# Kernel tuning notes

Hardware: AMD Instinct MI355X
Metric: run time of the kernel (lower is better)

The kernel has to match this reference:

```python
import jax, jax.numpy as jnp
import numpy as np

B, N, D, DH = 2, 512, 64, 64


def _lin_params(key, din, dout):
    kw, kb = jax.random.split(key)
    bound = 1.0 / np.sqrt(din)
    W = jax.random.uniform(kw, (din, dout), jnp.float32, -bound, bound)
    b = jax.random.uniform(kb, (dout,), jnp.float32, -bound, bound)
    return W, b


def setup_inputs() -> dict:
    key = jax.random.key(0)
    ks = jax.random.split(key, 11)
    inp = {
        "x": jax.random.normal(ks[0], (B, N, D), jnp.float32),
        "e": jax.random.normal(ks[1], (B, N, N, D), jnp.float32),
    }
    # node-to-node self-attention: Linear(d, d_head)
    inp["Wq1"], inp["bq1"] = _lin_params(ks[2], D, DH)
    inp["Wk1"], inp["bk1"] = _lin_params(ks[3], D, DH)
    inp["Wv1"], inp["bv1"] = _lin_params(ks[4], D, DH)
    # node-to-edge cross-attention
    inp["Wqe"], inp["bqe"] = _lin_params(ks[5], D, DH)   # Q_edge: Linear(d, d_head) on e
    inp["Wkn"], inp["bkn"] = _lin_params(ks[6], DH, DH)  # K_node: Linear(d_head, d_head)
    inp["Wvn"], inp["bvn"] = _lin_params(ks[7], DH, DH)  # V_node
    # edge-to-node cross-attention (all Linear(d_head, d_head))
    inp["Wqn"], inp["bqn"] = _lin_params(ks[8], DH, DH)
    inp["Wke"], inp["bke"] = _lin_params(ks[9], DH, DH)
    inp["Wve"], inp["bve"] = _lin_params(ks[10], DH, DH)
    return inp


def _forward(x, e, Wq1, bq1, Wk1, bk1, Wv1, bv1,
             Wqe, bqe, Wkn, bkn, Wvn, bvn,
             Wqn, bqn, Wke, bke, Wve, bve):
    sqrt_d = jnp.sqrt(jnp.asarray(DH, x.dtype))
    lin = lambda z, W, b: z @ W + b

    # --- self-attention node-to-node: x (B,N,d) -> x_hat (B,N,d_head) ---
    Q = lin(x, Wq1, bq1)
    K = lin(x, Wk1, bk1)
    V = lin(x, Wv1, bv1)
    A = jax.nn.softmax(jnp.einsum('bnd,bmd->bnm', Q, K) / sqrt_d, axis=-1)
    x_hat = jnp.einsum('bnm,bmd->bnd', A, V)

    # --- cross-attention node-to-edge: update e (B,N,N,d) -> e_new (B,N,N,d_head) ---
    Qe = lin(e, Wqe, bqe)                 # (B,N,N,dh)
    Kn = lin(x_hat, Wkn, bkn)             # (B,N,dh)
    Vn = lin(x_hat, Wvn, bvn)
    Si = jnp.einsum('bijd,bjd->bij', Qe, Kn) / sqrt_d  # K_i[b,i,j] = Kn[b,j]
    Sj = jnp.einsum('bijd,bid->bij', Qe, Kn) / sqrt_d  # K_j[b,i,j] = Kn[b,i]
    # Att_i/(Att_i+Att_j) = sigmoid(Si - Sj)
    Ai = jax.nn.sigmoid(Si - Sj)
    Aj = 1.0 - Ai
    e_new = Ai[..., None] * Vn[:, None, :, :] + Aj[..., None] * Vn[:, :, None, :]

    # --- cross-attention edge-to-node: x_new (B,N,d_head) ---
    Qn = lin(x_hat, Wqn, bqn)             # (B,N,dh)
    Ke = lin(e_new, Wke, bke)             # (B,N,N,dh)
    Ve = lin(e_new, Wve, bve)
    S = jnp.einsum('bid,bijd->bij', Qn, Ke) / sqrt_d
    A2 = jax.nn.softmax(S, axis=2)
    x_new = jnp.einsum('bij,bijd->bid', A2, Ve)
    return x_new, e_new


def reference(x, e, Wq1, bq1, Wk1, bk1, Wv1, bv1,
              Wqe, bqe, Wkn, bkn, Wvn, bvn,
              Wqn, bqn, Wke, bke, Wve, bve):
    return _forward(x, e, Wq1, bq1, Wk1, bk1, Wv1, bv1,
                    Wqe, bqe, Wkn, bkn, Wvn, bvn,
                    Wqn, bqn, Wke, bke, Wve, bve)
```

## Files before the change

### kernel.cpp

```cpp
#include <hip/hip_runtime.h>
#include <math.h>

#define NN 512

typedef float f4 __attribute__((ext_vector_type(4)));

__global__ __launch_bounds__(256) void prep_kernel(
    const float* __restrict__ x,
    const float* __restrict__ Wq1, const float* __restrict__ bq1,
    const float* __restrict__ Wk1, const float* __restrict__ bk1,
    const float* __restrict__ Wv1, const float* __restrict__ bv1,
    const float* __restrict__ Wkn, const float* __restrict__ bkn,
    const float* __restrict__ Wvn, const float* __restrict__ bvn,
    const float* __restrict__ Wqe, const float* __restrict__ bqe,
    const float* __restrict__ Wke, const float* __restrict__ Wve,
    float* __restrict__ Q, float* __restrict__ K, float* __restrict__ V,
    float* __restrict__ M_P, float* __restrict__ c_P,
    float* __restrict__ M_ke, float* __restrict__ c_ke,
    float* __restrict__ M_ve, float* __restrict__ c_ve,
    float* __restrict__ vq0, float* __restrict__ s0p)
{
    __shared__ float sh[14528];
    const int t = threadIdx.x;

    if (blockIdx.x < 3) {
        const int m = blockIdx.x;
        float* As = sh;
        float* Bs = sh + 4160;
        float* va = sh + 8320;
        float* vb = sh + 8384;
        const float* A  = (m == 0) ? Wkn : Wvn;
        const float* aV = (m == 0) ? bkn : bvn;
        const float* B  = (m == 0) ? Wqe : (m == 1 ? Wke : Wve);
#pragma unroll
        for (int p = 0; p < 16; ++p) {
            const int idx = p * 256 + t;
            const int r = idx >> 6, cc = idx & 63;
            As[r * 65 + cc] = A[idx];
            if (m == 0) Bs[r * 65 + cc] = B[idx];
            else        Bs[cc * 65 + r] = B[idx];
        }
        if (t < 64) { va[t] = aV[t]; vb[t] = bqe[t]; }
        __syncthreads();

        const int b = t & 63, g = t >> 6;
        float acc[16];
#pragma unroll
        for (int aa = 0; aa < 16; ++aa) acc[aa] = 0.f;
        for (int k = 0; k < 64; ++k) {
            const float bv = Bs[b * 65 + k];
#pragma unroll
            for (int aa = 0; aa < 16; ++aa)
                acc[aa] = fmaf(As[(g * 16 + aa) * 65 + k], bv, acc[aa]);
        }
        float* M = (m == 0) ? M_P : (m == 1 ? M_ke : M_ve);
#pragma unroll
        for (int aa = 0; aa < 16; ++aa)
            M[(g * 16 + aa) * 64 + b] = acc[aa];

        if (t < 64) {
            float cb = 0.f;
            for (int k = 0; k < 64; ++k) cb = fmaf(va[k], Bs[t * 65 + k], cb);
            float* C = (m == 0) ? c_P : (m == 1 ? c_ke : c_ve);
            C[t] = cb;
            if (m == 0) {
                float q = 0.f;
                for (int k = 0; k < 64; ++k) q = fmaf(As[t * 65 + k], vb[k], q);
                vq0[t] = q * 0.125f;
            }
        }
        if (m == 0 && t == 0) {
            float s = 0.f;
            for (int k = 0; k < 64; ++k) s += vb[k] * va[k];
            *s0p = s * 0.125f;
        }
    } else {
        const int rb = (blockIdx.x - 3) * 32;
        float* Ws0 = sh;
        float* Ws1 = sh + 4096;
        float* Ws2 = sh + 8192;
        float* xs  = sh + 12288;
        float* bs0 = sh + 14336;
        float* bs1 = sh + 14400;
        float* bs2 = sh + 14464;
#pragma unroll
        for (int p = 0; p < 4; ++p) {
            const int idx = p * 256 + t;
            ((f4*)Ws0)[idx] = ((const f4*)Wq1)[idx];
            ((f4*)Ws1)[idx] = ((const f4*)Wk1)[idx];
            ((f4*)Ws2)[idx] = ((const f4*)Wv1)[idx];
        }
        ((f4*)xs)[t]       = ((const f4*)(x + rb * 64))[t];
        ((f4*)xs)[t + 256] = ((const f4*)(x + rb * 64))[t + 256];
        if (t < 64) { bs0[t] = bq1[t]; bs1[t] = bk1[t]; bs2[t] = bv1[t]; }
        __syncthreads();

        const int d = t & 63, g = t >> 6;
        float a0[8], a1[8], a2[8];
#pragma unroll
        for (int r = 0; r < 8; ++r) { a0[r] = bs0[d]; a1[r] = bs1[d]; a2[r] = bs2[d]; }
        for (int k4 = 0; k4 < 16; ++k4) {
            float w0[4], w1[4], w2[4];
#pragma unroll
            for (int kk = 0; kk < 4; ++kk) {
                w0[kk] = Ws0[(k4 * 4 + kk) * 64 + d];
                w1[kk] = Ws1[(k4 * 4 + kk) * 64 + d];
                w2[kk] = Ws2[(k4 * 4 + kk) * 64 + d];
            }
#pragma unroll
            for (int r = 0; r < 8; ++r) {
                const f4 xv = ((const f4*)xs)[(g * 8 + r) * 16 + k4];
                a0[r] = fmaf(xv.x, w0[0], fmaf(xv.y, w0[1], fmaf(xv.z, w0[2], fmaf(xv.w, w0[3], a0[r]))));
                a1[r] = fmaf(xv.x, w1[0], fmaf(xv.y, w1[1], fmaf(xv.z, w1[2], fmaf(xv.w, w1[3], a1[r]))));
                a2[r] = fmaf(xv.x, w2[0], fmaf(xv.y, w2[1], fmaf(xv.z, w2[2], fmaf(xv.w, w2[3], a2[r]))));
            }
        }
#pragma unroll
        for (int r = 0; r < 8; ++r) {
            Q[(rb + g * 8 + r) * 64 + d] = a0[r];
            K[(rb + g * 8 + r) * 64 + d] = a1[r];
            V[(rb + g * 8 + r) * 64 + d] = a2[r];
        }
    }
}

__global__ __launch_bounds__(512) void selfattn_kernel(
    const float* __restrict__ Q, const float* __restrict__ K,
    const float* __restrict__ V, float* __restrict__ xhat)
{
    const int row = blockIdx.x;
    const int b = row >> 9;
    const int t = threadIdx.x;
    __shared__ float qr[64];
    __shared__ float p[512];
    __shared__ float red[512];
    if (t < 64) qr[t] = Q[row * 64 + t];
    __syncthreads();

    {
        const int m = t;
        const f4* kr = (const f4*)(K + (size_t)(b * NN + m) * 64);
        const f4* qq = (const f4*)qr;
        float sp[4] = {0.f, 0.f, 0.f, 0.f};
#pragma unroll
        for (int u = 0; u < 16; ++u) {
            const f4 w = kr[u];
            const f4 qv = qq[u];
            sp[u & 3] += qv.x * w.x + qv.y * w.y + qv.z * w.z + qv.w * w.w;
        }
        p[m] = ((sp[0] + sp[1]) + (sp[2] + sp[3])) * 0.125f;
    }
    __syncthreads();

    const int lane = t & 63, w = t >> 6;
    const float v0 = p[t];
    float m = v0;
#pragma unroll
    for (int o = 1; o < 64; o <<= 1) m = fmaxf(m, __shfl_xor(m, o));
    if (lane == 0) red[w] = m;
    __syncthreads();
    float mx = red[0];
#pragma unroll
    for (int z = 1; z < 8; ++z) mx = fmaxf(mx, red[z]);
    const float e0 = expf(v0 - mx);
    float ss = e0;
#pragma unroll
    for (int o = 1; o < 64; o <<= 1) ss += __shfl_xor(ss, o);
    if (lane == 0) red[8 + w] = ss;
    __syncthreads();
    const float inv = 1.f / (red[8] + red[9] + red[10] + red[11]
                           + red[12] + red[13] + red[14] + red[15]);
    p[t] = e0;
    __syncthreads();

    const int d = t & 63, q = t >> 6;
    float acc = 0.f;
    const int j0 = q * 64;
    for (int j = j0; j < j0 + 64; ++j)
        acc = fmaf(p[j], V[(b * NN + j) * 64 + d], acc);
    red[t] = acc;
    __syncthreads();
    if (t < 64) {
        float s8 = 0.f;
#pragma unroll
        for (int z = 0; z < 8; ++z) s8 += red[t + z * 64];
        xhat[row * 64 + t] = s8 * inv;
    }
}

__global__ __launch_bounds__(256) void affine5_kernel(
    const float* __restrict__ xhat,
    const float* __restrict__ Wqn, const float* __restrict__ bqn,
    const float* __restrict__ Wvn, const float* __restrict__ bvn,
    const float* __restrict__ M_P, const float* __restrict__ c_P,
    const float* __restrict__ M_ke, const float* __restrict__ c_ke,
    const float* __restrict__ M_ve, const float* __restrict__ c_ve,
    const float* __restrict__ vq0, const float* __restrict__ s0p,
    float* __restrict__ Qn, float* __restrict__ Vn, float* __restrict__ P,
    float* __restrict__ VnWke, float* __restrict__ VnWve, float* __restrict__ q0)
{
    const int t = threadIdx.x;
    const int rb = blockIdx.x * 32;
    const int m = blockIdx.y;
    const float* W; const float* c; float* o;
    if (m == 0)      { W = Wqn;  c = bqn;  o = Qn; }
    else if (m == 1) { W = Wvn;  c = bvn;  o = Vn; }
    else if (m == 2) { W = M_P;  c = c_P;  o = P; }
    else if (m == 3) { W = M_ke; c = c_ke; o = VnWke; }
    else             { W = M_ve; c = c_ve; o = VnWve; }
    __shared__ float Ws[4096], xs[2048], cs[64], vq0s[64];
#pragma unroll
    for (int p = 0; p < 4; ++p) ((f4*)Ws)[p * 256 + t] = ((const f4*)W)[p * 256 + t];
    ((f4*)xs)[t]       = ((const f4*)(xhat + rb * 64))[t];
    ((f4*)xs)[t + 256] = ((const f4*)(xhat + rb * 64))[t + 256];
    if (t < 64) { cs[t] = c[t]; if (m == 0) vq0s[t] = vq0[t]; }
    __syncthreads();

    const int d = t & 63, g = t >> 6;
    float acc[8];
#pragma unroll
    for (int r = 0; r < 8; ++r) acc[r] = cs[d];
    for (int k4 = 0; k4 < 16; ++k4) {
        float w[4];
#pragma unroll
        for (int kk = 0; kk < 4; ++kk) w[kk] = Ws[(k4 * 4 + kk) * 64 + d];
#pragma unroll
        for (int r = 0; r < 8; ++r) {
            const f4 xv = ((const f4*)xs)[(g * 8 + r) * 16 + k4];
            acc[r] = fmaf(xv.x, w[0], fmaf(xv.y, w[1], fmaf(xv.z, w[2], fmaf(xv.w, w[3], acc[r]))));
        }
    }
#pragma unroll
    for (int r = 0; r < 8; ++r) o[(rb + g * 8 + r) * 64 + d] = acc[r];

    if (m == 0) {
        const int row = t >> 3, seg = t & 7;
        float part = 0.f;
#pragma unroll
        for (int kk = 0; kk < 8; ++kk)
            part = fmaf(xs[row * 64 + seg * 8 + kk], vq0s[seg * 8 + kk], part);
        part += __shfl_xor(part, 1);
        part += __shfl_xor(part, 2);
        part += __shfl_xor(part, 4);
        if (seg == 0) q0[rb + row] = part + s0p[0];
    }
}

__global__ __launch_bounds__(256) void edgenode_kernel(
    const float* __restrict__ e, const float* __restrict__ P,
    const float* __restrict__ q0, const float* __restrict__ Vn,
    const float* __restrict__ Qn, const float* __restrict__ VnWke,
    const float* __restrict__ VnWve, const float* __restrict__ bve,
    float* __restrict__ e_new, float* __restrict__ x_new)
{
    const int bi = blockIdx.x;
    const int b = bi >> 9, i = bi & 511;
    const int t = threadIdx.x;
    const int r = t >> 4;
    const int k = t & 15;

    __shared__ float qn[64], pis[64], vis[64];
    __shared__ float as_[512], us[512], cs[512], q0s[512];
    __shared__ float red[256];

    if (t < 64) {
        qn[t]  = Qn[bi * 64 + t];
        pis[t] = P[bi * 64 + t];
        vis[t] = Vn[bi * 64 + t];
    }
    q0s[t]       = q0[b * NN + t];
    q0s[t + 256] = q0[b * NN + t + 256];
    __syncthreads();
    const float q0i = q0s[i];
    const float4 pi4 = ((const float4*)pis)[k];
    const float4 vi4 = ((const float4*)vis)[k];
    const float4 qn4 = ((const float4*)qn)[k];

    const f4* erow  = (const f4*)(e     + (size_t)bi * NN * 64);
    f4*       enrow = (f4*)      (e_new + (size_t)bi * NN * 64);

    for (int c0 = 0; c0 < 32; ++c0) {
        const int j  = c0 * 16 + r;
        const int bj = b * NN + j;
        const f4 ev = erow[j * 16 + k];
        const float4 pj = ((const float4*)P)[bj * 16 + k];
        const float4 wj = ((const float4*)VnWke)[bj * 16 + k];
        float s = ev.x * (pj.x - pi4.x) + ev.y * (pj.y - pi4.y)
                + ev.z * (pj.z - pi4.z) + ev.w * (pj.w - pi4.w);
        float uu = qn4.x * wj.x + qn4.y * wj.y + qn4.z * wj.z + qn4.w * wj.w;
        s  += __shfl_xor(s, 1);  uu += __shfl_xor(uu, 1);
        s  += __shfl_xor(s, 2);  uu += __shfl_xor(uu, 2);
        s  += __shfl_xor(s, 4);  uu += __shfl_xor(uu, 4);
        s  += __shfl_xor(s, 8);  uu += __shfl_xor(uu, 8);
        const float ai = 1.f / (1.f + expf(-(s * 0.125f + q0s[j] - q0i)));
        const float4 vj = ((const float4*)Vn)[bj * 16 + k];
        f4 en;
        en.x = fmaf(ai, vj.x - vi4.x, vi4.x);
        en.y = fmaf(ai, vj.y - vi4.y, vi4.y);
        en.z = fmaf(ai, vj.z - vi4.z, vi4.z);
        en.w = fmaf(ai, vj.w - vi4.w, vi4.w);
        __builtin_nontemporal_store(en, enrow + j * 16 + k);
        if (k == 0) { as_[j] = ai; us[j] = uu * 0.125f; }
    }
    __syncthreads();

    const int lane = t & 63, w = t >> 6;
    const float uii = us[i];
    const float v0 = as_[t] * (us[t] - uii);
    const float v1 = as_[t + 256] * (us[t + 256] - uii);
    float m = fmaxf(v0, v1);
#pragma unroll
    for (int o = 1; o < 64; o <<= 1) m = fmaxf(m, __shfl_xor(m, o));
    if (lane == 0) red[w] = m;
    __syncthreads();
    const float mx = fmaxf(fmaxf(red[0], red[1]), fmaxf(red[2], red[3]));
    const float e0 = expf(v0 - mx), e1 = expf(v1 - mx);
    float ss = e0 + e1;
#pragma unroll
    for (int o = 1; o < 64; o <<= 1) ss += __shfl_xor(ss, o);
    if (lane == 0) red[4 + w] = ss;
    __syncthreads();
    const float inv = 1.f / (red[4] + red[5] + red[6] + red[7]);
    const float c0v = e0 * inv * as_[t];
    const float c1v = e1 * inv * as_[t + 256];
    cs[t] = c0v; cs[t + 256] = c1v;
    float gg = c0v + c1v;
#pragma unroll
    for (int o = 1; o < 64; o <<= 1) gg += __shfl_xor(gg, o);
    if (lane == 0) red[8 + w] = gg;
    __syncthreads();
    const float g = red[8] + red[9] + red[10] + red[11];
    __syncthreads();

    const int d = t & 63, q = t >> 6;
    float acc = 0.f;
    const int j0 = q * 128;
    for (int j = j0; j < j0 + 128; ++j)
        acc = fmaf(cs[j], VnWve[(b * NN + j) * 64 + d], acc);
    red[t] = acc;
    __syncthreads();
    if (t < 64) {
        const float s4 = red[t] + red[t + 64] + red[t + 128] + red[t + 192];
        x_new[bi * 64 + t] = bve[t] + VnWve[bi * 64 + t] * (1.f - g) + s4;
    }
}

extern "C" void kernel_launch(void* const* d_in, const int* in_sizes, int n_in,
                              void* d_out, int out_size, void* d_ws, size_t ws_size,
                              hipStream_t stream) {
    const float* x   = (const float*)d_in[0];
    const float* e   = (const float*)d_in[1];
    const float* Wq1 = (const float*)d_in[2];  const float* bq1 = (const float*)d_in[3];
    const float* Wk1 = (const float*)d_in[4];  const float* bk1 = (const float*)d_in[5];
    const float* Wv1 = (const float*)d_in[6];  const float* bv1 = (const float*)d_in[7];
    const float* Wqe = (const float*)d_in[8];  const float* bqe = (const float*)d_in[9];
    const float* Wkn = (const float*)d_in[10]; const float* bkn = (const float*)d_in[11];
    const float* Wvn = (const float*)d_in[12]; const float* bvn = (const float*)d_in[13];
    const float* Wqn = (const float*)d_in[14]; const float* bqn = (const float*)d_in[15];
    const float* Wke = (const float*)d_in[16];
    const float* Wve = (const float*)d_in[18]; const float* bve = (const float*)d_in[19];

    float* out = (float*)d_out;
    float* x_new = out;
    float* e_new = out + 2 * NN * 64;

    float* ws = (float*)d_ws;
    const int R = 2 * NN;
    float* Q     = ws;
    float* K     = Q + R * 64;
    float* V     = K + R * 64;
    float* xhat  = V + R * 64;
    float* Qn    = xhat + R * 64;
    float* Vn    = Qn + R * 64;
    float* P     = Vn + R * 64;
    float* VnWke = P + R * 64;
    float* VnWve = VnWke + R * 64;
    float* q0    = VnWve + R * 64;
    float* M_P   = q0 + R;
    float* M_ke  = M_P + 4096;
    float* M_ve  = M_ke + 4096;
    float* c_P   = M_ve + 4096;
    float* c_ke  = c_P + 64;
    float* c_ve  = c_ke + 64;
    float* vq0   = c_ve + 64;
    float* s0    = vq0 + 64;

    prep_kernel<<<35, 256, 0, stream>>>(x, Wq1, bq1, Wk1, bk1, Wv1, bv1,
                                        Wkn, bkn, Wvn, bvn, Wqe, bqe, Wke, Wve,
                                        Q, K, V,
                                        M_P, c_P, M_ke, c_ke, M_ve, c_ve, vq0, s0);
    selfattn_kernel<<<R, 512, 0, stream>>>(Q, K, V, xhat);
    affine5_kernel<<<dim3(32, 5), 256, 0, stream>>>(xhat, Wqn, bqn, Wvn, bvn,
                                                    M_P, c_P, M_ke, c_ke, M_ve, c_ve,
                                                    vq0, s0,
                                                    Qn, Vn, P, VnWke, VnWve, q0);
    edgenode_kernel<<<R, 256, 0, stream>>>(e, P, q0, Vn, Qn, VnWke, VnWve, bve,
                                           e_new, x_new);
}
```

Baseline: 97.91 us.

## Split edge kernel over j-chunks and finish softmax reduction in a separate kernel

The per-row edge kernel is split into 8 blocks per (b,i), each handling 64 columns j. The softmax over j is computed without max subtraction, so partial exp sums, gated sums and weighted VnWve sums can be accumulated per chunk and combined by a small final kernel. This gives eight times more blocks to hide memory latency on the large e stream and removes the shared-memory serial dot-product phase. The cost is an extra launch, partial-sum workspace traffic, and possible overflow because the softmax is no longer max-stabilised.

```diff
diff --git a/kernel.cpp b/kernel.cpp
--- a/kernel.cpp
+++ b/kernel.cpp
@@ -2,6 +2,7 @@
 #include <math.h>
 
 #define NN 512
+#define RR 1024
 
 typedef float f4 __attribute__((ext_vector_type(4)));
 
@@ -246,45 +247,51 @@
     }
 }
 
-__global__ __launch_bounds__(256) void edgenode_kernel(
+__global__ __launch_bounds__(256) void edge_kernel(
     const float* __restrict__ e, const float* __restrict__ P,
     const float* __restrict__ q0, const float* __restrict__ Vn,
     const float* __restrict__ Qn, const float* __restrict__ VnWke,
-    const float* __restrict__ VnWve, const float* __restrict__ bve,
-    float* __restrict__ e_new, float* __restrict__ x_new)
+    const float* __restrict__ VnWve,
+    float* __restrict__ e_new,
+    float* __restrict__ Epart, float* __restrict__ Gpart, float* __restrict__ Wpart)
 {
-    const int bi = blockIdx.x;
-    const int b = bi >> 9, i = bi & 511;
-    const int t = threadIdx.x;
-    const int r = t >> 4;
-    const int k = t & 15;
-
-    __shared__ float qn[64], pis[64], vis[64];
-    __shared__ float as_[512], us[512], cs[512], q0s[512];
-    __shared__ float red[256];
-
-    if (t < 64) {
-        qn[t]  = Qn[bi * 64 + t];
-        pis[t] = P[bi * 64 + t];
-        vis[t] = Vn[bi * 64 + t];
-    }
-    q0s[t]       = q0[b * NN + t];
-    q0s[t + 256] = q0[b * NN + t + 256];
-    __syncthreads();
-    const float q0i = q0s[i];
-    const float4 pi4 = ((const float4*)pis)[k];
-    const float4 vi4 = ((const float4*)vis)[k];
-    const float4 qn4 = ((const float4*)qn)[k];
+    const int blk = blockIdx.x;
+    const int bi = blk >> 3;
+    const int jc = blk & 7;
+    const int b  = bi >> 9;
+    const int t  = threadIdx.x;
+    const int r  = t >> 4;
+    const int k  = t & 15;
+
+    const float q0i = q0[bi];
+    const f4 pi4 = ((const f4*)P)[bi * 16 + k];
+    const f4 vi4 = ((const f4*)Vn)[bi * 16 + k];
+    const f4 qn4 = ((const f4*)Qn)[bi * 16 + k];
+    const f4 wi4 = ((const f4*)VnWke)[bi * 16 + k];
+    float uii = qn4.x * wi4.x + qn4.y * wi4.y + qn4.z * wi4.z + qn4.w * wi4.w;
+    uii += __shfl_xor(uii, 1);
+    uii += __shfl_xor(uii, 2);
+    uii += __shfl_xor(uii, 4);
+    uii += __shfl_xor(uii, 8);
+    uii *= 0.125f;
 
     const f4* erow  = (const f4*)(e     + (size_t)bi * NN * 64);
     f4*       enrow = (f4*)      (e_new + (size_t)bi * NN * 64);
-
-    for (int c0 = 0; c0 < 32; ++c0) {
-        const int j  = c0 * 16 + r;
-        const int bj = b * NN + j;
+    const f4* Prow  = (const f4*)P     + (size_t)b * NN * 16;
+    const f4* Vrow  = (const f4*)Vn    + (size_t)b * NN * 16;
+    const f4* Krow  = (const f4*)VnWke + (size_t)b * NN * 16;
+    const f4* Wvrow = (const f4*)VnWve + (size_t)b * NN * 16;
+    const float* q0b = q0 + b * NN;
+
+    float Eacc = 0.f, Gacc = 0.f;
+    f4 Wacc = {0.f, 0.f, 0.f, 0.f};
+
+#pragma unroll
+    for (int it = 0; it < 4; ++it) {
+        const int j = jc * 64 + it * 16 + r;
         const f4 ev = erow[j * 16 + k];
-        const float4 pj = ((const float4*)P)[bj * 16 + k];
-        const float4 wj = ((const float4*)VnWke)[bj * 16 + k];
+        const f4 pj = Prow[j * 16 + k];
+        const f4 wj = Krow[j * 16 + k];
         float s = ev.x * (pj.x - pi4.x) + ev.y * (pj.y - pi4.y)
                 + ev.z * (pj.z - pi4.z) + ev.w * (pj.w - pi4.w);
         float uu = qn4.x * wj.x + qn4.y * wj.y + qn4.z * wj.z + qn4.w * wj.w;
@@ -292,57 +299,74 @@
         s  += __shfl_xor(s, 2);  uu += __shfl_xor(uu, 2);
         s  += __shfl_xor(s, 4);  uu += __shfl_xor(uu, 4);
         s  += __shfl_xor(s, 8);  uu += __shfl_xor(uu, 8);
-        const float ai = 1.f / (1.f + expf(-(s * 0.125f + q0s[j] - q0i)));
-        const float4 vj = ((const float4*)Vn)[bj * 16 + k];
+        const float ai = 1.f / (1.f + expf(-(s * 0.125f + q0b[j] - q0i)));
+        const f4 vj = Vrow[j * 16 + k];
         f4 en;
         en.x = fmaf(ai, vj.x - vi4.x, vi4.x);
         en.y = fmaf(ai, vj.y - vi4.y, vi4.y);
         en.z = fmaf(ai, vj.z - vi4.z, vi4.z);
         en.w = fmaf(ai, vj.w - vi4.w, vi4.w);
         __builtin_nontemporal_store(en, enrow + j * 16 + k);
-        if (k == 0) { as_[j] = ai; us[j] = uu * 0.125f; }
-    }
-    __syncthreads();
-
-    const int lane = t & 63, w = t >> 6;
-    const float uii = us[i];
-    const float v0 = as_[t] * (us[t] - uii);
-    const float v1 = as_[t + 256] * (us[t + 256] - uii);
-    float m = fmaxf(v0, v1);
-#pragma unroll
-    for (int o = 1; o < 64; o <<= 1) m = fmaxf(m, __shfl_xor(m, o));
-    if (lane == 0) red[w] = m;
-    __syncthreads();
-    const float mx = fmaxf(fmaxf(red[0], red[1]), fmaxf(red[2], red[3]));
-    const float e0 = expf(v0 - mx), e1 = expf(v1 - mx);
-    float ss = e0 + e1;
-#pragma unroll
-    for (int o = 1; o < 64; o <<= 1) ss += __shfl_xor(ss, o);
-    if (lane == 0) red[4 + w] = ss;
-    __syncthreads();
-    const float inv = 1.f / (red[4] + red[5] + red[6] + red[7]);
-    const float c0v = e0 * inv * as_[t];
-    const float c1v = e1 * inv * as_[t + 256];
-    cs[t] = c0v; cs[t + 256] = c1v;
-    float gg = c0v + c1v;
-#pragma unroll
-    for (int o = 1; o < 64; o <<= 1) gg += __shfl_xor(gg, o);
-    if (lane == 0) red[8 + w] = gg;
-    __syncthreads();
-    const float g = red[8] + red[9] + red[10] + red[11];
-    __syncthreads();
-
-    const int d = t & 63, q = t >> 6;
-    float acc = 0.f;
-    const int j0 = q * 128;
-    for (int j = j0; j < j0 + 128; ++j)
-        acc = fmaf(cs[j], VnWve[(b * NN + j) * 64 + d], acc);
-    red[t] = acc;
+
+        const float ex  = expf(ai * (uu * 0.125f - uii));
+        const float aex = ai * ex;
+        Eacc += ex;
+        Gacc += aex;
+        const f4 wv = Wvrow[j * 16 + k];
+        Wacc.x = fmaf(aex, wv.x, Wacc.x);
+        Wacc.y = fmaf(aex, wv.y, Wacc.y);
+        Wacc.z = fmaf(aex, wv.z, Wacc.z);
+        Wacc.w = fmaf(aex, wv.w, Wacc.w);
+    }
+
+    Eacc += __shfl_xor(Eacc, 16);  Eacc += __shfl_xor(Eacc, 32);
+    Gacc += __shfl_xor(Gacc, 16);  Gacc += __shfl_xor(Gacc, 32);
+    Wacc.x += __shfl_xor(Wacc.x, 16);  Wacc.x += __shfl_xor(Wacc.x, 32);
+    Wacc.y += __shfl_xor(Wacc.y, 16);  Wacc.y += __shfl_xor(Wacc.y, 32);
+    Wacc.z += __shfl_xor(Wacc.z, 16);  Wacc.z += __shfl_xor(Wacc.z, 32);
+    Wacc.w += __shfl_xor(Wacc.w, 16);  Wacc.w += __shfl_xor(Wacc.w, 32);
+
+    __shared__ float Wred[4][65];
+    __shared__ float EG[8];
+    const int l = t & 63, w = t >> 6;
+    if (l < 16) {
+        Wred[w][l * 4 + 0] = Wacc.x;
+        Wred[w][l * 4 + 1] = Wacc.y;
+        Wred[w][l * 4 + 2] = Wacc.z;
+        Wred[w][l * 4 + 3] = Wacc.w;
+        if (l == 0) { EG[w] = Eacc; EG[4 + w] = Gacc; }
+    }
     __syncthreads();
     if (t < 64) {
-        const float s4 = red[t] + red[t + 64] + red[t + 128] + red[t + 192];
-        x_new[bi * 64 + t] = bve[t] + VnWve[bi * 64 + t] * (1.f - g) + s4;
-    }
+        const float Wsum = Wred[0][t] + Wred[1][t] + Wred[2][t] + Wred[3][t];
+        Wpart[((size_t)jc * RR + bi) * 64 + t] = Wsum;
+        if (t == 0) {
+            Epart[jc * RR + bi] = EG[0] + EG[1] + EG[2] + EG[3];
+            Gpart[jc * RR + bi] = EG[4] + EG[5] + EG[6] + EG[7];
+        }
+    }
+}
+
+__global__ __launch_bounds__(64) void final_kernel(
+    const float* __restrict__ Epart, const float* __restrict__ Gpart,
+    const float* __restrict__ Wpart, const float* __restrict__ VnWve,
+    const float* __restrict__ bve, float* __restrict__ x_new)
+{
+    const int bi = blockIdx.x;
+    const int t = threadIdx.x;
+    float Wsum = 0.f;
+#pragma unroll
+    for (int jc = 0; jc < 8; ++jc)
+        Wsum += Wpart[((size_t)jc * RR + bi) * 64 + t];
+    float E = 0.f, G = 0.f;
+#pragma unroll
+    for (int jc = 0; jc < 8; ++jc) {
+        E += Epart[jc * RR + bi];
+        G += Gpart[jc * RR + bi];
+    }
+    const float inv = 1.f / E;
+    x_new[(size_t)bi * 64 + t] = bve[t] + VnWve[(size_t)bi * 64 + t] * (1.f - G * inv)
+                               + Wsum * inv;
 }
 
 extern "C" void kernel_launch(void* const* d_in, const int* in_sizes, int n_in,
@@ -365,18 +389,17 @@
     float* e_new = out + 2 * NN * 64;
 
     float* ws = (float*)d_ws;
-    const int R = 2 * NN;
     float* Q     = ws;
-    float* K     = Q + R * 64;
-    float* V     = K + R * 64;
-    float* xhat  = V + R * 64;
-    float* Qn    = xhat + R * 64;
-    float* Vn    = Qn + R * 64;
-    float* P     = Vn + R * 64;
-    float* VnWke = P + R * 64;
-    float* VnWve = VnWke + R * 64;
-    float* q0    = VnWve + R * 64;
-    float* M_P   = q0 + R;
+    float* K     = Q + RR * 64;
+    float* V     = K + RR * 64;
+    float* xhat  = V + RR * 64;
+    float* Qn    = xhat + RR * 64;
+    float* Vn    = Qn + RR * 64;
+    float* P     = Vn + RR * 64;
+    float* VnWke = P + RR * 64;
+    float* VnWve = VnWke + RR * 64;
+    float* q0    = VnWve + RR * 64;
+    float* M_P   = q0 + RR;
     float* M_ke  = M_P + 4096;
     float* M_ve  = M_ke + 4096;
     float* c_P   = M_ve + 4096;
@@ -384,16 +407,20 @@
     float* c_ve  = c_ke + 64;
     float* vq0   = c_ve + 64;
     float* s0    = vq0 + 64;
+    float* Epart = s0 + 64;
+    float* Gpart = Epart + 8 * RR;
+    float* Wpart = Gpart + 8 * RR;
 
     prep_kernel<<<35, 256, 0, stream>>>(x, Wq1, bq1, Wk1, bk1, Wv1, bv1,
                                         Wkn, bkn, Wvn, bvn, Wqe, bqe, Wke, Wve,
                                         Q, K, V,
                                         M_P, c_P, M_ke, c_ke, M_ve, c_ve, vq0, s0);
-    selfattn_kernel<<<R, 512, 0, stream>>>(Q, K, V, xhat);
+    selfattn_kernel<<<RR, 512, 0, stream>>>(Q, K, V, xhat);
     affine5_kernel<<<dim3(32, 5), 256, 0, stream>>>(xhat, Wqn, bqn, Wvn, bvn,
                                                     M_P, c_P, M_ke, c_ke, M_ve, c_ve,
                                                     vq0, s0,
                                                     Qn, Vn, P, VnWke, VnWve, q0);
-    edgenode_kernel<<<R, 256, 0, stream>>>(e, P, q0, Vn, Qn, VnWke, VnWve, bve,
-                                           e_new, x_new);
-}
+    edge_kernel<<<RR * 8, 256, 0, stream>>>(e, P, q0, Vn, Qn, VnWke, VnWve,
+                                            e_new, Epart, Gpart, Wpart);
+    final_kernel<<<RR, 64, 0, stream>>>(Epart, Gpart, Wpart, VnWve, bve, x_new);
+}
```

Measured after the change: 95.11 us. 1.03x faster.
